# Kernel tuning notes

Hardware: AMD Instinct MI355X
Metric: run time of the kernel (lower is better)

## Reference

```python
import jax, jax.numpy as jnp
import numpy as np

N = 4096  # num_neurons
THRESHOLD = 0.0  # torch forward default


def setup_inputs() -> dict:
    key = jax.random.key(0)
    k1, k2 = jax.random.split(key)
    W = jax.random.normal(k1, (N, N), dtype=jnp.float32)
    # Hopfield weights have zero self-connections (fill_diagonal_(0))
    W = W * (1.0 - jnp.eye(N, dtype=jnp.float32))
    x = jax.random.normal(k2, (N,), dtype=jnp.float32)
    return {"input_pattern": x, "weights": W, "max_iterations": 4}


def reference(input_pattern, weights, max_iterations):
    n = weights.shape[0]

    # One asynchronous neuron update: uses the CURRENT (partially updated) state.
    def neuron_step(state, i):
        activation = jnp.dot(weights[i], state)  # row-i dot current state
        state = state.at[i].set(jnp.sign(activation - THRESHOLD))
        return state, None

    # One full sweep over all neurons, in order 0..n-1 (asynchronous updates).
    def sweep(state, _):
        state, _ = jax.lax.scan(neuron_step, state, jnp.arange(n))
        return state, None

    # Fixed number of sweeps. A converged state is a fixed point of `sweep`,
    # so this matches the torch early-break loop's final output exactly.
    state, _ = jax.lax.scan(sweep, input_pattern, None, length=max_iterations)
    return state
```

## Files before the change

kernel.cpp:

```cpp
#include <hip/hip_runtime.h>

#define NN 4096
#define BB 128
#define GG 32
#define MAXT 8
#define MAXE (MAXT * GG)

__global__ __launch_bounds__(256)
void hop_init(const float* __restrict__ x, const float* __restrict__ W,
              int* __restrict__ flags, float* __restrict__ partial_buf)
{
    const int tid = threadIdx.x, bid = blockIdx.x;
    const int lane = tid & 63, w = tid >> 6;
    const int lam = lane & 31, half = lane >> 5;

    if (bid == 0 && tid < MAXE) flags[tid] = 0;

    const int tm = bid >> 3, tc = bid & 7;
    const int rbase = tm * BB, cbase = tc * 512;

    float4 xv[4];
#pragma unroll
    for (int u = 0; u < 4; ++u)
        xv[u] = *(const float4*)(x + cbase + 4 * lam + 128 * u);

#pragma unroll 2
    for (int it = 0; it < 16; ++it) {
        const int r = w * 32 + it * 2 + half;
        const float* wrow = W + (size_t)(rbase + r) * NN + cbase;
        float p = 0.f;
#pragma unroll
        for (int u = 0; u < 4; ++u) {
            float4 wv = *(const float4*)(wrow + 4 * lam + 128 * u);
            p = fmaf(wv.x, xv[u].x, p); p = fmaf(wv.y, xv[u].y, p);
            p = fmaf(wv.z, xv[u].z, p); p = fmaf(wv.w, xv[u].w, p);
        }
#pragma unroll
        for (int s = 16; s; s >>= 1) p += __shfl_xor(p, s);
        if (lam == 0) partial_buf[(size_t)bid * BB + r] = p;
    }
}

__global__ __launch_bounds__(256)
void hop_main(const float* __restrict__ x, const float* __restrict__ W,
              const int* __restrict__ maxit, float* __restrict__ out,
              int* __restrict__ flags, float* __restrict__ delta_buf,
              const float* __restrict__ partial_buf)
{
    __shared__ float wdT[BB][BB + 1];
    __shared__ float a_lds[BB];
    __shared__ float delta_lds[BB];
    __shared__ int   status_lds;

    const int tid = threadIdx.x;
    const int m = blockIdx.x;
    const int lane = tid & 63, w = tid >> 6;
    const int lam = lane & 31, half = lane >> 5;
    const int bm = m * BB;

    int T = *maxit; if (T > MAXT) T = MAXT; if (T < 0) T = 0;
    const long long tstart = clock64();

    for (int l = tid; l < BB * BB; l += 256) {
        const int i = l >> 7, j = l & 127;
        wdT[j][i] = W[(size_t)(bm + i) * NN + bm + j];
    }
    if (tid < BB) {
        float s = 0.f;
#pragma unroll
        for (int c = 0; c < 8; ++c) s += partial_buf[(size_t)(m * 8 + c) * BB + tid];
        a_lds[tid] = s;
    }
    float sold0 = 0.f, sold1 = 0.f;
    if (w == 0) { sold0 = x[bm + lane]; sold1 = x[bm + 64 + lane]; }
    __syncthreads();

    for (int e = 0; e < T * GG; ++e) {
        const int k = e & (GG - 1);
        if (k != m) {
            float4 wpre[16];
#pragma unroll
            for (int it = 0; it < 16; ++it) {
                const int r = w * 32 + it * 2 + half;
                wpre[it] = *(const float4*)(W + (size_t)(bm + r) * NN + k * BB + 4 * lam);
            }
            int fl;
            do {
                fl = __hip_atomic_load(&flags[e], __ATOMIC_ACQUIRE, __HIP_MEMORY_SCOPE_AGENT);
                if (fl) break;
                __builtin_amdgcn_s_sleep(1);
            } while ((clock64() - tstart) < 1000000000LL);
            if (fl == 1) {
                const float* db = delta_buf + (size_t)e * BB;
                const float4 d4 = *(const float4*)(db + 4 * lam);
#pragma unroll
                for (int it = 0; it < 16; ++it) {
                    const int r = w * 32 + it * 2 + half;
                    const float4 wv = wpre[it];
                    float p = fmaf(wv.x, d4.x, fmaf(wv.y, d4.y, fmaf(wv.z, d4.z, wv.w * d4.w)));
#pragma unroll
                    for (int s = 16; s; s >>= 1) p += __shfl_xor(p, s);
                    if (lam == 0) a_lds[r] += p;
                }
            }
        } else {
            __syncthreads();
            if (w == 0) {
                float c0 = a_lds[lane], c1 = a_lds[lane + 64];
                const float dp0 = 1.f - sold0, dm0 = -1.f - sold0;
                const float dp1 = 1.f - sold1, dm1 = -1.f - sold1;
                const float cand0 = c0 > 0.f ? dp0 : dm0;
                const float cand1 = c1 > 0.f ? dp1 : dm1;
                const unsigned long long bz = __ballot((cand0 != 0.f) || (cand1 != 0.f));
                float vdf0 = 0.f, vdf1 = 0.f;
                const int zero_all = (bz == 0ULL);
                if (!zero_all) {
                    float vsn0 = sold0, vsn1 = sold1;
                    float pw0[6], pw1[6];
#pragma unroll
                    for (int u = 0; u < 6; ++u) { pw0[u] = wdT[u][lane]; pw1[u] = wdT[u][lane + 64]; }
#pragma unroll
                    for (int j = 0; j < 64; ++j) {
                        const float dq = c0 > 0.f ? dp0 : dm0;
                        const float sq = c0 > 0.f ? 1.f : -1.f;
                        const float bc = __int_as_float(
                            __builtin_amdgcn_readlane(__float_as_int(dq), j));
                        const bool me = (lane == j);
                        vdf0 = me ? dq : vdf0;
                        vsn0 = me ? sq : vsn0;
                        const float w0 = pw0[j % 6], w1 = pw1[j % 6];
                        pw0[j % 6] = wdT[j + 6][lane];
                        pw1[j % 6] = wdT[j + 6][lane + 64];
                        c0 = fmaf(w0, bc, c0);
                        c1 = fmaf(w1, bc, c1);
                    }
                    const float cnd1 = c1 > 0.f ? dp1 : dm1;
                    const unsigned long long bz1 = __ballot(cnd1 != 0.f);
                    if (bz1 != 0ULL) {
#pragma unroll
                        for (int j = 64; j < 128; ++j) {
                            const float dq = c1 > 0.f ? dp1 : dm1;
                            const float sq = c1 > 0.f ? 1.f : -1.f;
                            const float bc = __int_as_float(
                                __builtin_amdgcn_readlane(__float_as_int(dq), j & 63));
                            const bool me = (lane == (j & 63));
                            vdf1 = me ? dq : vdf1;
                            vsn1 = me ? sq : vsn1;
                            const float w1 = pw1[j % 6];
                            if (j + 6 < BB) pw1[j % 6] = wdT[j + 6][lane + 64];
                            c1 = fmaf(w1, bc, c1);
                        }
                    }
                    sold0 = vsn0;
                    sold1 = vsn1;
                }
                if (lane == 0) status_lds = zero_all;
                if (!zero_all) {
                    delta_lds[lane] = vdf0;
                    delta_lds[lane + 64] = vdf1;
                    float* db = delta_buf + (size_t)e * BB;
                    db[lane] = vdf0;
                    db[lane + 64] = vdf1;
                }
                __threadfence();
                if (lane == 0)
                    __hip_atomic_store(&flags[e], zero_all ? 2 : 1,
                                       __ATOMIC_RELEASE, __HIP_MEMORY_SCOPE_AGENT);
            }
            __syncthreads();
            if (!status_lds) {
                float dv[4];
#pragma unroll
                for (int u = 0; u < 4; ++u) dv[u] = delta_lds[lam + 32 * u];
#pragma unroll 2
                for (int it = 0; it < 16; ++it) {
                    const int r = w * 32 + it * 2 + half;
                    float p = 0.f;
#pragma unroll
                    for (int u = 0; u < 4; ++u) p = fmaf(wdT[lam + 32 * u][r], dv[u], p);
#pragma unroll
                    for (int s = 16; s; s >>= 1) p += __shfl_xor(p, s);
                    if (lam == 0) a_lds[r] += p;
                }
            }
        }
    }

    if (w == 0) {
        out[bm + lane] = sold0;
        out[bm + 64 + lane] = sold1;
    }
}

extern "C" void kernel_launch(void* const* d_in, const int* in_sizes, int n_in,
                              void* d_out, int out_size, void* d_ws, size_t ws_size,
                              hipStream_t stream) {
    const float* x = (const float*)d_in[0];
    const float* W = (const float*)d_in[1];
    const int* maxit = (const int*)d_in[2];
    float* out = (float*)d_out;

    char* ws = (char*)d_ws;
    int* flags = (int*)ws;
    float* delta_buf = (float*)(ws + 1024);
    float* partial_buf = (float*)(ws + 1024 + (size_t)MAXE * BB * 4);
    if (ws_size < (size_t)(1024 + 2 * MAXE * BB * 4)) return;

    hipLaunchKernelGGL(hop_init, dim3(256), dim3(256), 0, stream,
                       x, W, flags, partial_buf);

    void* args[7];
    args[0] = (void*)&x; args[1] = (void*)&W; args[2] = (void*)&maxit;
    args[3] = (void*)&out; args[4] = (void*)&flags; args[5] = (void*)&delta_buf;
    args[6] = (void*)&partial_buf;
    (void)hipLaunchCooperativeKernel(hop_main, dim3(GG), dim3(256), args, 0u, stream);
}
```

Measured before the change: 1.189 ms.

## Publish block sign states as self-validating bitmask slots instead of delta+flag

The owner block now packs its 128 new signs into three 64-bit words, each carrying a top valid bit, and writes them with relaxed atomic stores. This replaces the float delta buffer, the thread fence and the release flag. Consumers poll all three words until every valid bit is set, then rebuild the delta from a per-block LDS copy of the previous state. The goal is to cut cross-block signalling latency on the serial critical path by removing the fence and the separate payload read. In exchange it adds a 16KB LDS state copy, an extra __syncthreads per epoch, and bit-unpacking work.

```diff
diff --git a/kernel.cpp b/kernel.cpp
--- a/kernel.cpp
+++ b/kernel.cpp
@@ -5,16 +5,21 @@
 #define GG 32
 #define MAXT 8
 #define MAXE (MAXT * GG)
+#define MASK63 0x7FFFFFFFFFFFFFFFull
+#define MASK62 0x3FFFFFFFFFFFFFFFull
+#define TOPBIT 0x8000000000000000ull
 
 __global__ __launch_bounds__(256)
 void hop_init(const float* __restrict__ x, const float* __restrict__ W,
-              int* __restrict__ flags, float* __restrict__ partial_buf)
+              unsigned long long* __restrict__ slots, float* __restrict__ partial_buf)
 {
     const int tid = threadIdx.x, bid = blockIdx.x;
     const int lane = tid & 63, w = tid >> 6;
     const int lam = lane & 31, half = lane >> 5;
 
-    if (bid == 0 && tid < MAXE) flags[tid] = 0;
+    if (bid == 0) {
+        for (int i = tid; i < MAXE * 8; i += 256) slots[i] = 0ull;
+    }
 
     const int tm = bid >> 3, tc = bid & 7;
     const int rbase = tm * BB, cbase = tc * 512;
@@ -44,13 +49,15 @@
 __global__ __launch_bounds__(256)
 void hop_main(const float* __restrict__ x, const float* __restrict__ W,
               const int* __restrict__ maxit, float* __restrict__ out,
-              int* __restrict__ flags, float* __restrict__ delta_buf,
+              unsigned long long* __restrict__ slots,
               const float* __restrict__ partial_buf)
 {
     __shared__ float wdT[BB][BB + 1];
     __shared__ float a_lds[BB];
+    __shared__ float prev_lds[NN];
     __shared__ float delta_lds[BB];
     __shared__ int   status_lds;
+    __shared__ int   nzw[2][4];
 
     const int tid = threadIdx.x;
     const int m = blockIdx.x;
@@ -65,6 +72,7 @@
         const int i = l >> 7, j = l & 127;
         wdT[j][i] = W[(size_t)(bm + i) * NN + bm + j];
     }
+    for (int i = tid; i < NN; i += 256) prev_lds[i] = x[i];
     if (tid < BB) {
         float s = 0.f;
 #pragma unroll
@@ -84,15 +92,40 @@
                 const int r = w * 32 + it * 2 + half;
                 wpre[it] = *(const float4*)(W + (size_t)(bm + r) * NN + k * BB + 4 * lam);
             }
-            int fl;
-            do {
-                fl = __hip_atomic_load(&flags[e], __ATOMIC_ACQUIRE, __HIP_MEMORY_SCOPE_AGENT);
-                if (fl) break;
+            const unsigned long long* sl = slots + (size_t)e * 8;
+            unsigned long long q0, q1, q2;
+            int iters = 0;
+            for (;;) {
+                q0 = __hip_atomic_load(&sl[0], __ATOMIC_RELAXED, __HIP_MEMORY_SCOPE_AGENT);
+                q1 = __hip_atomic_load(&sl[1], __ATOMIC_RELAXED, __HIP_MEMORY_SCOPE_AGENT);
+                q2 = __hip_atomic_load(&sl[2], __ATOMIC_RELAXED, __HIP_MEMORY_SCOPE_AGENT);
+                if ((q0 & q1 & q2) >> 63) break;
                 __builtin_amdgcn_s_sleep(1);
-            } while ((clock64() - tstart) < 1000000000LL);
-            if (fl == 1) {
-                const float* db = delta_buf + (size_t)e * BB;
-                const float4 d4 = *(const float4*)(db + 4 * lam);
+                if (((++iters) & 255) == 0 && (clock64() - tstart) > 2000000000LL) break;
+            }
+            const unsigned long long m0 = (q0 & MASK63) | (q1 << 63);
+            const unsigned long long m1 = ((q1 >> 1) & MASK62) | (q2 << 62);
+
+            const int jc = 4 * lam;
+            const float4 pv = *(const float4*)&prev_lds[k * BB + jc];
+            float4 d4;
+            {
+                const float s0 = ((jc + 0 < 64 ? (m0 >> (jc + 0)) : (m1 >> (jc - 64))) & 1) ? 1.f : -1.f;
+                const float s1 = ((jc + 1 < 64 ? (m0 >> (jc + 1)) : (m1 >> (jc - 63))) & 1) ? 1.f : -1.f;
+                const float s2 = ((jc + 2 < 64 ? (m0 >> (jc + 2)) : (m1 >> (jc - 62))) & 1) ? 1.f : -1.f;
+                const float s3 = ((jc + 3 < 64 ? (m0 >> (jc + 3)) : (m1 >> (jc - 61))) & 1) ? 1.f : -1.f;
+                d4.x = s0 - pv.x; d4.y = s1 - pv.y; d4.z = s2 - pv.z; d4.w = s3 - pv.w;
+            }
+            const bool nz = (d4.x != 0.f) || (d4.y != 0.f) || (d4.z != 0.f) || (d4.w != 0.f);
+            const unsigned long long bnz = __ballot(nz);
+            if (lane == 0) nzw[e & 1][w] = (bnz != 0ull);
+            __syncthreads();
+            if (tid < BB) {
+                const int b = tid < 64 ? (int)((m0 >> tid) & 1) : (int)((m1 >> (tid - 64)) & 1);
+                prev_lds[k * BB + tid] = b ? 1.f : -1.f;
+            }
+            const int any = nzw[e & 1][0] | nzw[e & 1][1] | nzw[e & 1][2] | nzw[e & 1][3];
+            if (any) {
 #pragma unroll
                 for (int it = 0; it < 16; ++it) {
                     const int r = w * 32 + it * 2 + half;
@@ -154,18 +187,24 @@
                     sold0 = vsn0;
                     sold1 = vsn1;
                 }
+                {
+                    const unsigned long long m0 = __ballot(sold0 > 0.f);
+                    const unsigned long long m1 = __ballot(sold1 > 0.f);
+                    unsigned long long* sl = slots + (size_t)e * 8;
+                    if (lane == 0) {
+                        __hip_atomic_store(&sl[0], TOPBIT | (m0 & MASK63),
+                                           __ATOMIC_RELAXED, __HIP_MEMORY_SCOPE_AGENT);
+                        __hip_atomic_store(&sl[1], TOPBIT | (m0 >> 63) | ((m1 & MASK62) << 1),
+                                           __ATOMIC_RELAXED, __HIP_MEMORY_SCOPE_AGENT);
+                        __hip_atomic_store(&sl[2], TOPBIT | (m1 >> 62),
+                                           __ATOMIC_RELAXED, __HIP_MEMORY_SCOPE_AGENT);
+                    }
+                }
                 if (lane == 0) status_lds = zero_all;
                 if (!zero_all) {
                     delta_lds[lane] = vdf0;
                     delta_lds[lane + 64] = vdf1;
-                    float* db = delta_buf + (size_t)e * BB;
-                    db[lane] = vdf0;
-                    db[lane + 64] = vdf1;
-                }
-                __threadfence();
-                if (lane == 0)
-                    __hip_atomic_store(&flags[e], zero_all ? 2 : 1,
-                                       __ATOMIC_RELEASE, __HIP_MEMORY_SCOPE_AGENT);
+                }
             }
             __syncthreads();
             if (!status_lds) {
@@ -201,17 +240,15 @@
     float* out = (float*)d_out;
 
     char* ws = (char*)d_ws;
-    int* flags = (int*)ws;
-    float* delta_buf = (float*)(ws + 1024);
-    float* partial_buf = (float*)(ws + 1024 + (size_t)MAXE * BB * 4);
-    if (ws_size < (size_t)(1024 + 2 * MAXE * BB * 4)) return;
+    unsigned long long* slots = (unsigned long long*)ws;
+    float* partial_buf = (float*)(ws + (size_t)MAXE * 8 * 8);
+    if (ws_size < (size_t)(MAXE * 64 + 256 * BB * 4)) return;
 
     hipLaunchKernelGGL(hop_init, dim3(256), dim3(256), 0, stream,
-                       x, W, flags, partial_buf);
-
-    void* args[7];
+                       x, W, slots, partial_buf);
+
+    void* args[6];
     args[0] = (void*)&x; args[1] = (void*)&W; args[2] = (void*)&maxit;
-    args[3] = (void*)&out; args[4] = (void*)&flags; args[5] = (void*)&delta_buf;
-    args[6] = (void*)&partial_buf;
+    args[3] = (void*)&out; args[4] = (void*)&slots; args[5] = (void*)&partial_buf;
     (void)hipLaunchCooperativeKernel(hop_main, dim3(GG), dim3(256), args, 0u, stream);
 }
```

After: 1.103 ms. 1.08x faster.
